# Kernel optimization log

Measured on AMD Instinct MI355X. Metric: run time of the kernel, lower is better.

Reference implementation:

```python
import jax, jax.numpy as jnp
from jax import lax
import numpy as np

FILTER_SIZE = 3
PAD = FILTER_SIZE // 2


def _smooth(off, filt):
    # ReflectionPad2d(pad) -> conv2d(padding=pad) -> crop pad:-pad  == same-size smoothing
    x = jnp.pad(off, ((0, 0), (0, 0), (PAD, PAD), (PAD, PAD)), mode='reflect')
    y = lax.conv_general_dilated(x, filt, window_strides=(1, 1),
                                 padding=[(PAD, PAD), (PAD, PAD)],
                                 dimension_numbers=('NCHW', 'OIHW', 'NCHW'))
    return y[:, :, PAD:-PAD, PAD:-PAD]


def _grid_sample(img, gx, gy):
    # img: [C,H,W]; gx,gy: [N,H,W] normalized to [-1,1].
    # Bilinear, align_corners=True, zero padding (torch 1.x default at repo time).
    C, H, W = img.shape
    ix = (gx + 1.0) * 0.5 * (W - 1)
    iy = (gy + 1.0) * 0.5 * (H - 1)
    x0 = jnp.floor(ix); y0 = jnp.floor(iy)
    x1 = x0 + 1.0;      y1 = y0 + 1.0
    wx1 = ix - x0; wx0 = 1.0 - wx1
    wy1 = iy - y0; wy0 = 1.0 - wy1

    def gather(xi, yi):
        valid = ((xi >= 0) & (xi <= W - 1) & (yi >= 0) & (yi <= H - 1)).astype(img.dtype)
        xc = jnp.clip(xi, 0, W - 1).astype(jnp.int32)
        yc = jnp.clip(yi, 0, H - 1).astype(jnp.int32)
        return img[:, yc, xc] * valid[None]  # [C,N,H,W]

    out = (gather(x0, y0) * (wx0 * wy0)[None] +
           gather(x1, y0) * (wx1 * wy0)[None] +
           gather(x0, y1) * (wx0 * wy1)[None] +
           gather(x1, y1) * (wx1 * wy1)[None])
    return out  # [C,N,H,W]


def setup_inputs() -> dict:
    key = jax.random.key(0)
    k1, k2, k3 = jax.random.split(key, 3)
    C, H, W = 16, 512, 960
    F2 = FILTER_SIZE * FILTER_SIZE
    right_input = jax.random.normal(k1, (1, C, H, W), jnp.float32)
    offset_x = jax.random.uniform(k2, (1, 1, H, W), jnp.float32) * 64.0  # disparity-like
    offset_y = jax.random.uniform(k3, (1, 1, H, W), jnp.float32) * 8.0
    x_coordinate = jnp.tile(jnp.arange(W, dtype=jnp.float32)[None, None, None, :], (1, 1, H, 1))
    y_coordinate = jnp.tile(jnp.arange(H, dtype=jnp.float32)[None, None, :, None], (1, 1, 1, W))
    # one-hot neighbour extraction filters: channel i picks neighbour i of the 3x3 patch
    neighbour_extraction_filter = jnp.eye(F2, dtype=jnp.float32).reshape(F2, 1, FILTER_SIZE, FILTER_SIZE)
    return {'right_input': right_input, 'offset_x': offset_x, 'offset_y': offset_y,
            'x_coordinate': x_coordinate, 'y_coordinate': y_coordinate,
            'neighbour_extraction_filter': neighbour_extraction_filter}


def reference(right_input, offset_x, offset_y, x_coordinate, y_coordinate, neighbour_extraction_filter):
    H, W = offset_x.shape[2], offset_x.shape[3]
    sx = _smooth(offset_x, neighbour_extraction_filter)  # [1,F2,H,W]
    sy = _smooth(offset_y, neighbour_extraction_filter)  # [1,F2,H,W]
    coord_x = jnp.clip(x_coordinate - sx, 0.0, W - 1)
    coord_y = jnp.clip(y_coordinate - sy, 0.0, H - 1)
    half_w = W / 2.0; half_h = H / 2.0
    gx = (coord_x - half_w) / half_w  # [1,F2,H,W]
    gy = (coord_y - half_h) / half_h
    # grid batch = 1*F2; instead of repeating right_input F2 times, gather from the
    # single image for all F2 grids at once, then patch-vote (mean over F2).
    rec = _grid_sample(right_input[0], gx[0], gy[0])  # [C,F2,H,W]
    return jnp.mean(rec, axis=1)[None]  # [1,C,H,W]
```

## Files before the change

### kernel.cpp

```cpp
#include <hip/hip_runtime.h>

#define CH 16
#define HH 512
#define WW 960
#define HW (HH * WW)

#define RROWS 18
#define RCOLS 136
#define NTASK (RROWS * 2 * RCOLS)

typedef float v2f __attribute__((ext_vector_type(2)));

__device__ __forceinline__ unsigned f2bf(float f) {
  const unsigned u = __float_as_uint(f);
  return (u + 0x7fffu + ((u >> 16) & 1u)) >> 16;
}

__global__ __launch_bounds__(1024, 8) void recon_fused(
    const float* __restrict__ img,
    const float* __restrict__ offx,
    const float* __restrict__ offy,
    float* __restrict__ out) {
  extern __shared__ uint4 lds[];

  const int hwid = blockIdx.x + blockIdx.y * 15;
  const int tile = (hwid & 7) * 120 + (hwid >> 3);
  const int tx   = tile % 15;
  const int ty   = tile / 15;
  const int x0b  = tx * 64;
  const int y0b  = ty * 8;
  const int tid  = threadIdx.x;

  const int ylo = y0b - 9;
  const int xlo = x0b - 68;

#pragma unroll
  for (int it = 0; it < 5; ++it) {
    const int f = it * 1024 + tid;
    if (f < NTASK) {
      const int col = f % RCOLS;
      const int rc  = f / RCOLS;
      const int chv = rc & 1;
      const int row = rc >> 1;
      const int gr  = min(max(ylo + row, 0), HH - 1);
      const int gc  = min(max(xlo + col, 0), WW - 1);
      const float* src = img + (chv * 8) * HW + gr * WW + gc;
      uint4 o;
      o.x = f2bf(src[0 * HW]) | (f2bf(src[1 * HW]) << 16);
      o.y = f2bf(src[2 * HW]) | (f2bf(src[3 * HW]) << 16);
      o.z = f2bf(src[4 * HW]) | (f2bf(src[5 * HW]) << 16);
      o.w = f2bf(src[6 * HW]) | (f2bf(src[7 * HW]) << 16);
      lds[(row * RCOLS + col) * 2 + chv] = o;
    }
  }
  __syncthreads();

  const int chunk = tid & 1;
  const int pixl  = (tid >> 1) & 63;
  const int rowl  = tid >> 7;
  const int x     = x0b + pixl;
  const int y     = y0b + rowl;

  const float fxs = (float)(WW - 1) / (float)WW;
  const float fys = (float)(HH - 1) / (float)HH;

  v2f a01 = {0.f, 0.f}, a23 = {0.f, 0.f}, a45 = {0.f, 0.f}, a67 = {0.f, 0.f};

#define ACC8(V, Wt)                                                       \
  {                                                                       \
    const v2f w2 = {(Wt), (Wt)};                                          \
    v2f t;                                                                \
    t = (v2f){__uint_as_float((V).x << 16),                               \
              __uint_as_float((V).x & 0xffff0000u)};                      \
    a01 = __builtin_elementwise_fma(w2, t, a01);                          \
    t = (v2f){__uint_as_float((V).y << 16),                               \
              __uint_as_float((V).y & 0xffff0000u)};                      \
    a23 = __builtin_elementwise_fma(w2, t, a23);                          \
    t = (v2f){__uint_as_float((V).z << 16),                               \
              __uint_as_float((V).z & 0xffff0000u)};                      \
    a45 = __builtin_elementwise_fma(w2, t, a45);                          \
    t = (v2f){__uint_as_float((V).w << 16),                               \
              __uint_as_float((V).w & 0xffff0000u)};                      \
    a67 = __builtin_elementwise_fma(w2, t, a67);                          \
  }

#pragma unroll
  for (int di = -1; di <= 1; ++di) {
    int rr = y + di;
    rr = (rr < 0) ? 1 : ((rr >= HH) ? (HH - 2) : rr);
#pragma unroll
    for (int dj = -1; dj <= 1; ++dj) {
      int cc = x + dj;
      cc = (cc < 0) ? 1 : ((cc >= WW) ? (WW - 2) : cc);
      const int o = rr * WW + cc;
      const float sx = offx[o];
      const float sy = offy[o];
      const float cx = fminf(fmaxf((float)x - sx, 0.0f), (float)(WW - 1));
      const float cy = fminf(fmaxf((float)y - sy, 0.0f), (float)(HH - 1));
      const float ix = cx * fxs;
      const float iy = cy * fys;
      const float fx0 = floorf(ix);
      const float fy0 = floorf(iy);
      const float wx1 = ix - fx0, wx0 = 1.0f - wx1;
      const float wy1 = iy - fy0, wy0 = 1.0f - wy1;
      const float w00 = wx0 * wy0, w10 = wx1 * wy0;
      const float w01 = wx0 * wy1, w11 = wx1 * wy1;

      const int ry = (int)fy0 - ylo;
      const int rx = (int)fx0 - xlo;
      const uint4* p = &lds[(ry * RCOLS + rx) * 2 + chunk];
      const uint4 v00 = p[0];
      const uint4 v10 = p[2];
      const uint4 v01 = p[2 * RCOLS];
      const uint4 v11 = p[2 * RCOLS + 2];

      ACC8(v00, w00)
      ACC8(v10, w10)
      ACC8(v01, w01)
      ACC8(v11, w11)
    }
  }
#undef ACC8

  const float s = 1.0f / 9.0f;
  const int po = y * WW + x;
  const int c0 = chunk * 8;
  out[(c0 + 0) * HW + po] = a01.x * s;
  out[(c0 + 1) * HW + po] = a01.y * s;
  out[(c0 + 2) * HW + po] = a23.x * s;
  out[(c0 + 3) * HW + po] = a23.y * s;
  out[(c0 + 4) * HW + po] = a45.x * s;
  out[(c0 + 5) * HW + po] = a45.y * s;
  out[(c0 + 6) * HW + po] = a67.x * s;
  out[(c0 + 7) * HW + po] = a67.y * s;
}

extern "C" void kernel_launch(void* const* d_in, const int* in_sizes, int n_in,
                              void* d_out, int out_size, void* d_ws, size_t ws_size,
                              hipStream_t stream) {
  const float* right = (const float*)d_in[0];
  const float* offx  = (const float*)d_in[1];
  const float* offy  = (const float*)d_in[2];
  float* out = (float*)d_out;

  const dim3 grid(WW / 64, HH / 8);
  const size_t lds_bytes = (size_t)RROWS * RCOLS * 2 * sizeof(uint4);
  recon_fused<<<grid, 1024, lds_bytes, stream>>>(right, offx, offy, out);
}
```

Baseline: 119.2 us.

## Store image tile as fp16 and accumulate with packed half FMAs per pixel

Converts the staged image tile to fp16 with pkrtz instead of bf16, and accumulates bilinear corners using packed half2 FMAs, flushing to fp32 accumulators once per filter row. Each thread now handles all 16 channels for one pixel, so blocks shrink to 512 threads and the offset loads and weight maths are no longer duplicated across two threads. The channel halves are read in alternating order by thread parity to spread LDS bank use. The aim is to cut ALU work and the redundant per-pixel coordinate computation. It risks fp16 range and precision loss, and needs more registers per thread.

```diff
diff --git a/kernel.cpp b/kernel.cpp
--- a/kernel.cpp
+++ b/kernel.cpp
@@ -1,93 +1,83 @@
 #include <hip/hip_runtime.h>
+#include <hip/hip_fp16.h>
 
 #define CH 16
 #define HH 512
 #define WW 960
 #define HW (HH * WW)
 
+#define TR 8
+#define TC 64
 #define RROWS 18
 #define RCOLS 136
-#define NTASK (RROWS * 2 * RCOLS)
+#define NHALF (RROWS * RCOLS * 2)
 
-typedef float v2f __attribute__((ext_vector_type(2)));
+typedef __fp16 v2hf __attribute__((ext_vector_type(2)));
+typedef _Float16 h2r __attribute__((ext_vector_type(2)));
 
-__device__ __forceinline__ unsigned f2bf(float f) {
-  const unsigned u = __float_as_uint(f);
-  return (u + 0x7fffu + ((u >> 16) & 1u)) >> 16;
+__device__ __forceinline__ unsigned pkrtz_u(float a, float b) {
+  v2hf r = __builtin_amdgcn_cvt_pkrtz(a, b);
+  return __builtin_bit_cast(unsigned, r);
+}
+__device__ __forceinline__ __half2 u2h(unsigned u) {
+  return __builtin_bit_cast(__half2, u);
 }
 
-__global__ __launch_bounds__(1024, 8) void recon_fused(
+__global__ __launch_bounds__(512, 4) void recon_fused_f16(
     const float* __restrict__ img,
     const float* __restrict__ offx,
     const float* __restrict__ offy,
     float* __restrict__ out) {
-  extern __shared__ uint4 lds[];
+  __shared__ uint4 lds[NHALF];
 
   const int hwid = blockIdx.x + blockIdx.y * 15;
   const int tile = (hwid & 7) * 120 + (hwid >> 3);
-  const int tx   = tile % 15;
-  const int ty   = tile / 15;
-  const int x0b  = tx * 64;
-  const int y0b  = ty * 8;
-  const int tid  = threadIdx.x;
+  const int tx = tile % 15, ty = tile / 15;
+  const int x0b = tx * TC, y0b = ty * TR;
+  const int tid = threadIdx.x;
+  const int ylo = y0b - 9, xlo = x0b - 68;
 
-  const int ylo = y0b - 9;
-  const int xlo = x0b - 68;
-
-#pragma unroll
-  for (int it = 0; it < 5; ++it) {
-    const int f = it * 1024 + tid;
-    if (f < NTASK) {
-      const int col = f % RCOLS;
-      const int rc  = f / RCOLS;
-      const int chv = rc & 1;
-      const int row = rc >> 1;
-      const int gr  = min(max(ylo + row, 0), HH - 1);
-      const int gc  = min(max(xlo + col, 0), WW - 1);
-      const float* src = img + (chv * 8) * HW + gr * WW + gc;
+  for (int it = 0; it < 10; ++it) {
+    const int f = it * 512 + tid;
+    if (f < NHALF) {
+      const int half = f & 1;
+      const int p    = f >> 1;
+      const int row  = p / RCOLS;
+      const int col  = p - row * RCOLS;
+      const int gr = min(max(ylo + row, 0), HH - 1);
+      const int gc = min(max(xlo + col, 0), WW - 1);
+      const float* src = img + (half * 8) * HW + gr * WW + gc;
       uint4 o;
-      o.x = f2bf(src[0 * HW]) | (f2bf(src[1 * HW]) << 16);
-      o.y = f2bf(src[2 * HW]) | (f2bf(src[3 * HW]) << 16);
-      o.z = f2bf(src[4 * HW]) | (f2bf(src[5 * HW]) << 16);
-      o.w = f2bf(src[6 * HW]) | (f2bf(src[7 * HW]) << 16);
-      lds[(row * RCOLS + col) * 2 + chv] = o;
+      o.x = pkrtz_u(src[0 * HW], src[1 * HW]);
+      o.y = pkrtz_u(src[2 * HW], src[3 * HW]);
+      o.z = pkrtz_u(src[4 * HW], src[5 * HW]);
+      o.w = pkrtz_u(src[6 * HW], src[7 * HW]);
+      lds[f] = o;
     }
   }
   __syncthreads();
 
-  const int chunk = tid & 1;
-  const int pixl  = (tid >> 1) & 63;
-  const int rowl  = tid >> 7;
-  const int x     = x0b + pixl;
-  const int y     = y0b + rowl;
+  const int pixl = tid & 63;
+  const int rowl = tid >> 6;
+  const int x = x0b + pixl;
+  const int y = y0b + rowl;
+  const int cA = tid & 1;
 
   const float fxs = (float)(WW - 1) / (float)WW;
   const float fys = (float)(HH - 1) / (float)HH;
 
-  v2f a01 = {0.f, 0.f}, a23 = {0.f, 0.f}, a45 = {0.f, 0.f}, a67 = {0.f, 0.f};
-
-#define ACC8(V, Wt)                                                       \
-  {                                                                       \
-    const v2f w2 = {(Wt), (Wt)};                                          \
-    v2f t;                                                                \
-    t = (v2f){__uint_as_float((V).x << 16),                               \
-              __uint_as_float((V).x & 0xffff0000u)};                      \
-    a01 = __builtin_elementwise_fma(w2, t, a01);                          \
-    t = (v2f){__uint_as_float((V).y << 16),                               \
-              __uint_as_float((V).y & 0xffff0000u)};                      \
-    a23 = __builtin_elementwise_fma(w2, t, a23);                          \
-    t = (v2f){__uint_as_float((V).z << 16),                               \
-              __uint_as_float((V).z & 0xffff0000u)};                      \
-    a45 = __builtin_elementwise_fma(w2, t, a45);                          \
-    t = (v2f){__uint_as_float((V).w << 16),                               \
-              __uint_as_float((V).w & 0xffff0000u)};                      \
-    a67 = __builtin_elementwise_fma(w2, t, a67);                          \
-  }
+  float accA[8], accB[8];
+#pragma unroll
+  for (int i = 0; i < 8; ++i) { accA[i] = 0.f; accB[i] = 0.f; }
 
 #pragma unroll
   for (int di = -1; di <= 1; ++di) {
     int rr = y + di;
     rr = (rr < 0) ? 1 : ((rr >= HH) ? (HH - 2) : rr);
+    __half2 hA[4], hB[4];
+#pragma unroll
+    for (int i = 0; i < 4; ++i) { hA[i] = u2h(0u); hB[i] = u2h(0u); }
+
 #pragma unroll
     for (int dj = -1; dj <= 1; ++dj) {
       int cc = x + dj;
@@ -103,36 +93,52 @@
       const float fy0 = floorf(iy);
       const float wx1 = ix - fx0, wx0 = 1.0f - wx1;
       const float wy1 = iy - fy0, wy0 = 1.0f - wy1;
-      const float w00 = wx0 * wy0, w10 = wx1 * wy0;
-      const float w01 = wx0 * wy1, w11 = wx1 * wy1;
+      const int u00 = ((int)fy0 - ylo) * RCOLS + ((int)fx0 - xlo);
 
-      const int ry = (int)fy0 - ylo;
-      const int rx = (int)fx0 - xlo;
-      const uint4* p = &lds[(ry * RCOLS + rx) * 2 + chunk];
-      const uint4 v00 = p[0];
-      const uint4 v10 = p[2];
-      const uint4 v01 = p[2 * RCOLS];
-      const uint4 v11 = p[2 * RCOLS + 2];
+      const __half2 w00 = u2h(pkrtz_u(wx0 * wy0, wx0 * wy0));
+      const __half2 w10 = u2h(pkrtz_u(wx1 * wy0, wx1 * wy0));
+      const __half2 w01 = u2h(pkrtz_u(wx0 * wy1, wx0 * wy1));
+      const __half2 w11 = u2h(pkrtz_u(wx1 * wy1, wx1 * wy1));
 
-      ACC8(v00, w00)
-      ACC8(v10, w10)
-      ACC8(v01, w01)
-      ACC8(v11, w11)
+#define CORNER(UIDX, Wh)                                     \
+  {                                                          \
+    const uint4 qa = lds[((UIDX) << 1) + cA];                \
+    const uint4 qb = lds[((UIDX) << 1) + (cA ^ 1)];          \
+    hA[0] = __hfma2(u2h(qa.x), (Wh), hA[0]);                 \
+    hA[1] = __hfma2(u2h(qa.y), (Wh), hA[1]);                 \
+    hA[2] = __hfma2(u2h(qa.z), (Wh), hA[2]);                 \
+    hA[3] = __hfma2(u2h(qa.w), (Wh), hA[3]);                 \
+    hB[0] = __hfma2(u2h(qb.x), (Wh), hB[0]);                 \
+    hB[1] = __hfma2(u2h(qb.y), (Wh), hB[1]);                 \
+    hB[2] = __hfma2(u2h(qb.z), (Wh), hB[2]);                 \
+    hB[3] = __hfma2(u2h(qb.w), (Wh), hB[3]);                 \
+  }
+      CORNER(u00, w00)
+      CORNER(u00 + 1, w10)
+      CORNER(u00 + RCOLS, w01)
+      CORNER(u00 + RCOLS + 1, w11)
+#undef CORNER
+    }
+#pragma unroll
+    for (int i = 0; i < 4; ++i) {
+      const h2r a = __builtin_bit_cast(h2r, hA[i]);
+      const h2r b = __builtin_bit_cast(h2r, hB[i]);
+      accA[2 * i]     += (float)a.x;
+      accA[2 * i + 1] += (float)a.y;
+      accB[2 * i]     += (float)b.x;
+      accB[2 * i + 1] += (float)b.y;
     }
   }
-#undef ACC8
 
   const float s = 1.0f / 9.0f;
   const int po = y * WW + x;
-  const int c0 = chunk * 8;
-  out[(c0 + 0) * HW + po] = a01.x * s;
-  out[(c0 + 1) * HW + po] = a01.y * s;
-  out[(c0 + 2) * HW + po] = a23.x * s;
-  out[(c0 + 3) * HW + po] = a23.y * s;
-  out[(c0 + 4) * HW + po] = a45.x * s;
-  out[(c0 + 5) * HW + po] = a45.y * s;
-  out[(c0 + 6) * HW + po] = a67.x * s;
-  out[(c0 + 7) * HW + po] = a67.y * s;
+#pragma unroll
+  for (int j = 0; j < 8; ++j) {
+    const float lo = (cA ? accB[j] : accA[j]) * s;
+    const float hi = (cA ? accA[j] : accB[j]) * s;
+    out[j * HW + po]       = lo;
+    out[(j + 8) * HW + po] = hi;
+  }
 }
 
 extern "C" void kernel_launch(void* const* d_in, const int* in_sizes, int n_in,
@@ -143,7 +149,6 @@
   const float* offy  = (const float*)d_in[2];
   float* out = (float*)d_out;
 
-  const dim3 grid(WW / 64, HH / 8);
-  const size_t lds_bytes = (size_t)RROWS * RCOLS * 2 * sizeof(uint4);
-  recon_fused<<<grid, 1024, lds_bytes, stream>>>(right, offx, offy, out);
+  const dim3 grid(WW / TC, HH / TR);
+  recon_fused_f16<<<grid, 512, 0, stream>>>(right, offx, offy, out);
 }
```

Measured after the change: 117.6 us. About the same (-1.3%).
